# Kernel tuning notes

Hardware: AMD Instinct MI355X
Metric: run time of the kernel (lower is better)

## Reference

```python
import jax, jax.numpy as jnp
import numpy as np
import math

N_HEAD = 9
N_KV_HEAD = 3
HEAD_DIM = 64
ROPE_THETA = 100000.0


def _rope_cos_sin(seq_len, dim, theta):
    inv_freq = 1.0 / (theta ** (jnp.arange(0, dim, 2, dtype=jnp.float32) / dim))  # (dim//2,)
    t = jnp.arange(seq_len, dtype=jnp.float32)
    ang = jnp.outer(t, inv_freq)  # (T, dim//2)
    return jnp.cos(ang), jnp.sin(ang)


def _apply_rope(x, cos, sin):
    # x: (B, H, T, D); pairs are interleaved along D (torch view_as_complex on (..., D//2, 2))
    B, H, T, D = x.shape
    xr = x.reshape(B, H, T, D // 2, 2)
    x0, x1 = xr[..., 0], xr[..., 1]
    c = cos[None, None, :, :]
    s = sin[None, None, :, :]
    out0 = x0 * c - x1 * s
    out1 = x0 * s + x1 * c
    return jnp.stack([out0, out1], axis=-1).reshape(B, H, T, D)


def setup_inputs() -> dict:
    key = jax.random.key(0)
    ks = jax.random.split(key, 5)
    B, T, C = 4, 2048, 576
    scale_in = 1.0 / math.sqrt(C)
    return {
        "x": jax.random.normal(ks[0], (B, T, C), dtype=jnp.float32),
        "wq": jax.random.normal(ks[1], (N_HEAD * HEAD_DIM, C), dtype=jnp.float32) * scale_in,
        "wk": jax.random.normal(ks[2], (N_KV_HEAD * HEAD_DIM, C), dtype=jnp.float32) * scale_in,
        "wv": jax.random.normal(ks[3], (N_KV_HEAD * HEAD_DIM, C), dtype=jnp.float32) * scale_in,
        "wo": jax.random.normal(ks[4], (C, N_HEAD * HEAD_DIM), dtype=jnp.float32) * scale_in,
    }


def reference(x, wq, wk, wv, wo):
    B, T, C = x.shape
    n_rep = N_HEAD // N_KV_HEAD

    q = (x @ wq.T).reshape(B, T, N_HEAD, HEAD_DIM).transpose(0, 2, 1, 3)      # (B,Hq,T,D)
    k = (x @ wk.T).reshape(B, T, N_KV_HEAD, HEAD_DIM).transpose(0, 2, 1, 3)   # (B,Hkv,T,D)
    v = (x @ wv.T).reshape(B, T, N_KV_HEAD, HEAD_DIM).transpose(0, 2, 1, 3)

    cos, sin = _rope_cos_sin(T, HEAD_DIM, ROPE_THETA)
    q = _apply_rope(q, cos, sin)
    k = _apply_rope(k, cos, sin)

    # GQA: broadcast each KV head across n_rep query heads without materializing copies
    qg = q.reshape(B, N_KV_HEAD, n_rep, T, HEAD_DIM)
    att = jnp.einsum("bgrtd,bgsd->bgrts", qg, k) * (1.0 / math.sqrt(HEAD_DIM))  # (B,Hkv,rep,T,T)
    causal = jnp.tril(jnp.ones((T, T), dtype=bool))
    att = jnp.where(causal[None, None, None, :, :], att, -jnp.inf)
    att = jax.nn.softmax(att, axis=-1)
    y = jnp.einsum("bgrts,bgsd->bgrtd", att, v)                                # (B,Hkv,rep,T,D)
    y = y.reshape(B, N_HEAD, T, HEAD_DIM).transpose(0, 2, 1, 3).reshape(B, T, N_HEAD * HEAD_DIM)
    return y @ wo.T
```

## Files before the change

kernel.cpp:

```cpp
#include <hip/hip_runtime.h>
#include <stdint.h>

typedef __attribute__((ext_vector_type(8))) short bf16x8;
typedef __attribute__((ext_vector_type(16))) float f32x16;

#define MFMA32(a, b, c) __builtin_amdgcn_mfma_f32_32x32x16_bf16(a, b, c, 0, 0, 0)

#define BB 4
#define TT 2048
#define CC 576
#define NH 9
#define NKV 3
#define HD 64
#define MM (BB * TT)
#define NQKV 960

#define QSC 0.18033688011112042f

__device__ __forceinline__ unsigned short f2bf(float f) {
  union { float f; uint32_t u; } v; v.f = f;
  uint32_t u = v.u;
  uint32_t r = (u + 0x7fffu + ((u >> 16) & 1u)) >> 16;
  return (unsigned short)r;
}

__device__ __forceinline__ void gl16(const void* g, void* l) {
  __builtin_amdgcn_global_load_lds(
      (const __attribute__((address_space(1))) unsigned int*)g,
      (__attribute__((address_space(3))) unsigned int*)l, 16, 0, 0);
}

__device__ __forceinline__ float fexp2(float x) {
  float r;
  asm("v_exp_f32 %0, %1" : "=v"(r) : "v"(x));
  return r;
}

__global__ __launch_bounds__(256) void prep_kernel(
    const float* __restrict__ x, const float* __restrict__ wq,
    const float* __restrict__ wk, const float* __restrict__ wv,
    const float* __restrict__ wo,
    unsigned short* __restrict__ xh, unsigned short* __restrict__ wqkv,
    unsigned short* __restrict__ woh, float* __restrict__ tc,
    float* __restrict__ ts) {
  const int NX4 = MM * CC / 4;
  const int NW4 = NQKV * CC / 4;
  const int NO4 = CC * CC / 4;
  const int NT = TT * 32;
  const int total = NX4 + NW4 + NO4 + NT;
  for (int i = blockIdx.x * blockDim.x + threadIdx.x; i < total;
       i += gridDim.x * blockDim.x) {
    if (i < NX4) {
      float4 v = ((const float4*)x)[i];
      ushort4 o;
      o.x = f2bf(v.x); o.y = f2bf(v.y); o.z = f2bf(v.z); o.w = f2bf(v.w);
      ((ushort4*)xh)[i] = o;
    } else if (i < NX4 + NW4) {
      int j = i - NX4;
      int n = (j * 4) / CC;
      const float* src = (n < 576) ? wq + j * 4
                       : (n < 768) ? wk + j * 4 - 576 * CC
                                   : wv + j * 4 - 768 * CC;
      float4 v = *(const float4*)src;
      ushort4 o;
      o.x = f2bf(v.x); o.y = f2bf(v.y); o.z = f2bf(v.z); o.w = f2bf(v.w);
      ((ushort4*)wqkv)[j] = o;
    } else if (i < NX4 + NW4 + NO4) {
      int j = i - NX4 - NW4;
      float4 v = ((const float4*)wo)[j];
      ushort4 o;
      o.x = f2bf(v.x); o.y = f2bf(v.y); o.z = f2bf(v.z); o.w = f2bf(v.w);
      ((ushort4*)woh)[j] = o;
    } else {
      int j = i - NX4 - NW4 - NO4;
      int t = j >> 5, pi = j & 31;
      double invf = pow(100000.0, -(double)(2 * pi) / 64.0);
      double ang = (double)t * invf;
      tc[j] = (float)cos(ang);
      ts[j] = (float)sin(ang);
    }
  }
}

__global__ __launch_bounds__(256) void gemm_qkv(
    const unsigned short* __restrict__ xh, const unsigned short* __restrict__ wqkv,
    const float* __restrict__ tc, const float* __restrict__ ts,
    unsigned short* __restrict__ qb, unsigned short* __restrict__ kst,
    unsigned short* __restrict__ vst) {
  const int l = threadIdx.x & 63, w = threadIdx.x >> 6;
  const int ln = l & 31, hi = l >> 5;
  const int bm = blockIdx.y * 128, bn = blockIdx.x * 64;

  __shared__ unsigned short als[2][8192];
  __shared__ unsigned short bls[2][4096];

  int asrc[4], bsrc[2];
#pragma unroll
  for (int i = 0; i < 4; ++i)
    asrc[i] = (bm + w * 32 + i * 8 + (l >> 3)) * CC + ((l & 7) ^ ((l >> 3) & 7)) * 8;
#pragma unroll
  for (int i = 0; i < 2; ++i)
    bsrc[i] = (bn + w * 16 + i * 8 + (l >> 3)) * CC + ((l & 7) ^ ((l >> 3) & 7)) * 8;

  f32x16 acc0, acc1;
#pragma unroll
  for (int r = 0; r < 16; ++r) { acc0[r] = 0.f; acc1[r] = 0.f; }

#pragma unroll
  for (int i = 0; i < 4; ++i) gl16(xh + asrc[i], (char*)&als[0][0] + w * 4096 + i * 1024);
#pragma unroll
  for (int i = 0; i < 2; ++i) gl16(wqkv + bsrc[i], (char*)&bls[0][0] + w * 2048 + i * 1024);

  int cur = 0;
  for (int t = 0; t < 9; ++t) {
    if (t + 1 < 9) {
      const int k0 = (t + 1) * 64;
#pragma unroll
      for (int i = 0; i < 4; ++i)
        gl16(xh + asrc[i] + k0, (char*)&als[cur ^ 1][0] + w * 4096 + i * 1024);
#pragma unroll
      for (int i = 0; i < 2; ++i)
        gl16(wqkv + bsrc[i] + k0, (char*)&bls[cur ^ 1][0] + w * 2048 + i * 1024);
      asm volatile("s_waitcnt vmcnt(6)" ::: "memory");
    } else {
      asm volatile("s_waitcnt vmcnt(0)" ::: "memory");
    }
    __builtin_amdgcn_s_barrier();
    __builtin_amdgcn_sched_barrier(0);

    const char* ab = (const char*)&als[cur][0];
    const char* bb = (const char*)&bls[cur][0];
    __builtin_amdgcn_s_setprio(1);
#pragma unroll
    for (int ks = 0; ks < 4; ++ks) {
      const int ch = (((ks * 2 + hi) ^ (ln & 7)) << 4);
      bf16x8 af = *(const bf16x8*)(ab + (w * 32 + ln) * 128 + ch);
      bf16x8 b0 = *(const bf16x8*)(bb + ln * 128 + ch);
      bf16x8 b1 = *(const bf16x8*)(bb + (32 + ln) * 128 + ch);
      acc0 = MFMA32(af, b0, acc0);
      acc1 = MFMA32(af, b1, acc1);
    }
    __builtin_amdgcn_s_setprio(0);

    __builtin_amdgcn_sched_barrier(0);
    __builtin_amdgcn_s_barrier();
    cur ^= 1;
  }

#pragma unroll
  for (int n32 = 0; n32 < 2; ++n32) {
    const int col = bn + n32 * 32 + ln;
    const int d = col & 63;
#pragma unroll
    for (int r = 0; r < 16; ++r) {
      const int m = bm + w * 32 + (r & 3) + 8 * (r >> 2) + 4 * hi;
      float v = n32 ? acc1[r] : acc0[r];
      float partner = __shfl_xor(v, 1);
      const int bi = m >> 11, t = m & 2047;
      if (col < 768) {
        const int pi = d >> 1;
        const float c = tc[t * 32 + pi], s = ts[t * 32 + pi];
        v = (d & 1) ? (partner * s + v * c) : (v * c - partner * s);
      }
      if (col < 576) {
        const int h = col >> 6;
        qb[(((size_t)bi * NH + h) * TT + t) * HD + d] = f2bf(v * QSC);
      } else if (col < 768) {
        const int h = (col - 576) >> 6;
        const size_t head = (size_t)bi * NKV + h;
        kst[((head * 32 + (t >> 6)) * 64 + (t & 63)) * 64 + (d ^ ((t & 7) << 3))] = f2bf(v);
      } else {
        const int h = (col - 768) >> 6;
        const size_t head = (size_t)bi * NKV + h;
        vst[((head * 32 + (t >> 6)) * 64 + d) * 64 + ((t & 63) ^ ((d & 7) << 3))] = f2bf(v);
      }
    }
  }
}

__global__ __launch_bounds__(512) void attn_kernel(
    const unsigned short* __restrict__ qbuf, const unsigned short* __restrict__ kst,
    const unsigned short* __restrict__ vst, unsigned short* __restrict__ yb) {
  const int j = blockIdx.x, kvh = blockIdx.y, b = blockIdx.z;
  const int i = j % 7, hr = j / 7;
  const int h = kvh * 3 + hr;
  const int l = threadIdx.x & 63;
  const int w8 = threadIdx.x >> 6;
  const int g = w8 >> 2;
  const int wq = w8 & 3;
  const int ln = l & 31, hi = l >> 5;
  const size_t head = (size_t)b * NKV + kvh;

  const int qt0 = 15 - i, qt1 = i + 2, qt2 = (i == 5) ? 0 : 1;
  const int m0 = qt0 + 1, m1 = qt1 + 1;
  const int m2 = (i >= 5) ? qt2 + 1 : 0;
  const int m01 = m0 + m1;
  const int tot = m01 + m2;

  __shared__ unsigned short kls[2][3][4096];
  __shared__ unsigned short vls[2][3][4096];
  __shared__ float licomb[256];

  const unsigned short* qptr = qbuf + ((size_t)b * NH + h) * TT * HD;
  const int row0 = qt0 * 128 + wq * 32 + ln;
  const int row1 = qt1 * 128 + wq * 32 + ln;
  const int row2 = qt2 * 128 + wq * 32 + ln;

  bf16x8 qf0[4], qf1[4], qf2[4], qc[4];
#pragma unroll
  for (int ds = 0; ds < 4; ++ds) {
    qf0[ds] = *(const bf16x8*)(qptr + (size_t)row0 * HD + ds * 16 + hi * 8);
    qf1[ds] = *(const bf16x8*)(qptr + (size_t)row1 * HD + ds * 16 + hi * 8);
    qf2[ds] = *(const bf16x8*)(qptr + (size_t)row2 * HD + ds * 16 + hi * 8);
  }
  qc[0] = qf0[0]; qc[1] = qf0[1]; qc[2] = qf0[2]; qc[3] = qf0[3];
  int qt_c = qt0, qrow_c = row0, nt_c = m0;

  const char* kgb = (const char*)(kst + head * 32 * 4096);
  const char* vgb = (const char*)(vst + head * 32 * 4096);

  f32x16 o0, o1, fzero;
  float ls[16];
#pragma unroll
  for (int r = 0; r < 16; ++r) { o0[r] = 0.f; o1[r] = 0.f; ls[r] = 0.f; fzero[r] = 0.f; }

#pragma unroll
  for (int pre = 0; pre < 2; ++pre) {
    const size_t tb = (size_t)(2 * pre + g) * 8192;
#pragma unroll
    for (int i2 = 0; i2 < 2; ++i2) {
      const int off = wq * 2048 + i2 * 1024;
      gl16(kgb + tb + off + l * 16, (char*)&kls[g][pre][0] + off);
      gl16(vgb + tb + off + l * 16, (char*)&vls[g][pre][0] + off);
    }
  }
  asm volatile("s_waitcnt vmcnt(4)" ::: "memory");
  __builtin_amdgcn_s_barrier();
  __builtin_amdgcn_sched_barrier(0);

  const int swz = (ln & 7) << 4;
  int jt = 0;
  int s = 0;

  for (int it = 0; it < tot; ++it) {
    if (it + 2 < tot) {
      const int f = it + 2;
      const int u2 = (f < m0) ? f : ((f < m01) ? f - m0 : f - m01);
      const size_t tb = (size_t)(2 * u2 + g) * 8192;
      char* kl = (char*)&kls[g][(it + 2) % 3][0];
      char* vl = (char*)&vls[g][(it + 2) % 3][0];
#pragma unroll
      for (int i2 = 0; i2 < 2; ++i2) {
        const int off = wq * 2048 + i2 * 1024;
        gl16(kgb + tb + off + l * 16, kl + off);
        gl16(vgb + tb + off + l * 16, vl + off);
      }
    }

    const char* kb = (const char*)&kls[g][it % 3][0];
    const char* vb = (const char*)&vls[g][it % 3][0];

    f32x16 s0, s1;
    __builtin_amdgcn_s_setprio(1);
    {
      const int cb0 = (hi * 16) ^ swz;
      bf16x8 k0 = *(const bf16x8*)(kb + ln * 128 + cb0);
      bf16x8 k1 = *(const bf16x8*)(kb + (32 + ln) * 128 + cb0);
      s0 = MFMA32(k0, qc[0], fzero);
      s1 = MFMA32(k1, qc[0], fzero);
    }
#pragma unroll
    for (int ds = 1; ds < 4; ++ds) {
      const int cb = (ds * 32 + hi * 16) ^ swz;
      bf16x8 k0 = *(const bf16x8*)(kb + ln * 128 + cb);
      bf16x8 k1 = *(const bf16x8*)(kb + (32 + ln) * 128 + cb);
      s0 = MFMA32(k0, qc[ds], s0);
      s1 = MFMA32(k1, qc[ds], s1);
    }
    __builtin_amdgcn_s_setprio(0);

    const bool segEnd = (jt == qt_c);
    if (segEnd) {
      const int kvt = 2 * qt_c + g;
#pragma unroll
      for (int r = 0; r < 16; ++r) {
        const int kg = kvt * 64 + (r & 3) + 8 * (r >> 2) + 4 * hi;
        if (kg > qrow_c) s0[r] = -1e30f;
        if (kg + 32 > qrow_c) s1[r] = -1e30f;
      }
    }

#pragma unroll
    for (int r = 0; r < 16; ++r) {
      s0[r] = fexp2(s0[r]);
      s1[r] = fexp2(s1[r]);
    }
#pragma unroll
    for (int r = 0; r < 16; ++r) ls[r] += s0[r] + s1[r];

    unsigned int pa[4][4];
#pragma unroll
    for (int t = 0; t < 2; ++t) {
#pragma unroll
      for (int m = 0; m < 2; ++m) {
        float p0 = t ? s1[8 * m + 0] : s0[8 * m + 0];
        float p1 = t ? s1[8 * m + 1] : s0[8 * m + 1];
        float p2 = t ? s1[8 * m + 2] : s0[8 * m + 2];
        float p3 = t ? s1[8 * m + 3] : s0[8 * m + 3];
        float p4 = t ? s1[8 * m + 4] : s0[8 * m + 4];
        float p5 = t ? s1[8 * m + 5] : s0[8 * m + 5];
        float p6 = t ? s1[8 * m + 6] : s0[8 * m + 6];
        float p7 = t ? s1[8 * m + 7] : s0[8 * m + 7];
        unsigned int w0, w1, w2, w3;
        asm("v_cvt_pk_bf16_f32 %0, %1, %2" : "=v"(w0) : "v"(p0), "v"(p1));
        asm("v_cvt_pk_bf16_f32 %0, %1, %2" : "=v"(w1) : "v"(p2), "v"(p3));
        asm("v_cvt_pk_bf16_f32 %0, %1, %2" : "=v"(w2) : "v"(p4), "v"(p5));
        asm("v_cvt_pk_bf16_f32 %0, %1, %2" : "=v"(w3) : "v"(p6), "v"(p7));
        asm("v_permlane32_swap_b32 %0, %1" : "+v"(w0), "+v"(w2));
        asm("v_permlane32_swap_b32 %0, %1" : "+v"(w1), "+v"(w3));
        pa[2 * t + m][0] = w0; pa[2 * t + m][1] = w1;
        pa[2 * t + m][2] = w2; pa[2 * t + m][3] = w3;
      }
    }

    __builtin_amdgcn_s_setprio(1);
#pragma unroll
    for (int ks = 0; ks < 4; ++ks) {
      union { unsigned int u[4]; bf16x8 v; } cvt;
      cvt.u[0] = pa[ks][0]; cvt.u[1] = pa[ks][1];
      cvt.u[2] = pa[ks][2]; cvt.u[3] = pa[ks][3];
      const int cb = (ks * 32 + hi * 16) ^ swz;
      bf16x8 v0 = *(const bf16x8*)(vb + ln * 128 + cb);
      bf16x8 v1 = *(const bf16x8*)(vb + (32 + ln) * 128 + cb);
      o0 = MFMA32(cvt.v, v0, o0);
      o1 = MFMA32(cvt.v, v1, o1);
    }
    __builtin_amdgcn_s_setprio(0);

    if (segEnd) {
      float tm0 = 0.f;
#pragma unroll
      for (int st = 8; st >= 1; st >>= 1)
#pragma unroll
        for (int r = 0; r < 8; ++r)
          if (r < st) ls[r] += ls[r + st];
      tm0 = ls[0] + __shfl_xor(ls[0], 32);
      char* chunk;
      {
        const int buf = it % 3;
        chunk = (char*)((wq == 0) ? &kls[0][buf][0]
               : (wq == 1) ? &vls[0][buf][0]
               : (wq == 2) ? &kls[1][buf][0]
                           : &vls[1][buf][0]);
      }
      __syncthreads();
      if (g == 1) {
#pragma unroll
        for (int r = 0; r < 16; ++r) {
          *(float*)(chunk + r * 256 + l * 4) = o0[r];
          *(float*)(chunk + (16 + r) * 256 + l * 4) = o1[r];
        }
        licomb[wq * 64 + l] = tm0;
      }
      __syncthreads();
      if (g == 0) {
#pragma unroll
        for (int r = 0; r < 16; ++r) {
          o0[r] += *(const float*)(chunk + r * 256 + l * 4);
          o1[r] += *(const float*)(chunk + (16 + r) * 256 + l * 4);
        }
        const float li = tm0 + licomb[wq * 64 + l];
        const float inv = 1.0f / li;
#pragma unroll
        for (int r = 0; r < 16; ++r) {
          const int cr = (r & 3) + 8 * (r >> 2) + 4 * hi;
          const float ir = __shfl(inv, cr);
          const int t = qt_c * 128 + wq * 32 + cr;
          unsigned short* yp = yb + ((size_t)b * TT + t) * CC + h * HD;
          yp[ln] = f2bf(o0[r] * ir);
          yp[32 + ln] = f2bf(o1[r] * ir);
        }
      }
#pragma unroll
      for (int r = 0; r < 16; ++r) { o0[r] = 0.f; o1[r] = 0.f; ls[r] = 0.f; }
    }

    __builtin_amdgcn_sched_barrier(0);
    if (it + 2 < tot) {
      asm volatile("s_waitcnt vmcnt(4)" ::: "memory");
    } else {
      asm volatile("s_waitcnt vmcnt(0)" ::: "memory");
    }
    __builtin_amdgcn_s_barrier();
    __builtin_amdgcn_sched_barrier(0);

    ++jt;
    if (jt == nt_c) {
      jt = 0; ++s;
      if (s == 1) {
        qt_c = qt1; qrow_c = row1; nt_c = m1;
        qc[0] = qf1[0]; qc[1] = qf1[1]; qc[2] = qf1[2]; qc[3] = qf1[3];
      } else {
        qt_c = qt2; qrow_c = row2; nt_c = m2;
        qc[0] = qf2[0]; qc[1] = qf2[1]; qc[2] = qf2[2]; qc[3] = qf2[3];
      }
    }
  }
}

__global__ __launch_bounds__(256) void gemm_out(
    const unsigned short* __restrict__ yb, const unsigned short* __restrict__ woh,
    float* __restrict__ out) {
  const int l = threadIdx.x & 63, w = threadIdx.x >> 6;
  const int ln = l & 31, hi = l >> 5;
  const int bm = blockIdx.y * 128, bn = blockIdx.x * 64;

  __shared__ unsigned short als[2][8192];
  __shared__ unsigned short bls[2][4096];

  int asrc[4], bsrc[2];
#pragma unroll
  for (int i = 0; i < 4; ++i)
    asrc[i] = (bm + w * 32 + i * 8 + (l >> 3)) * CC + ((l & 7) ^ ((l >> 3) & 7)) * 8;
#pragma unroll
  for (int i = 0; i < 2; ++i)
    bsrc[i] = (bn + w * 16 + i * 8 + (l >> 3)) * CC + ((l & 7) ^ ((l >> 3) & 7)) * 8;

  f32x16 acc0, acc1;
#pragma unroll
  for (int r = 0; r < 16; ++r) { acc0[r] = 0.f; acc1[r] = 0.f; }

#pragma unroll
  for (int i = 0; i < 4; ++i) gl16(yb + asrc[i], (char*)&als[0][0] + w * 4096 + i * 1024);
#pragma unroll
  for (int i = 0; i < 2; ++i) gl16(woh + bsrc[i], (char*)&bls[0][0] + w * 2048 + i * 1024);

  int cur = 0;
  for (int t = 0; t < 9; ++t) {
    if (t + 1 < 9) {
      const int k0 = (t + 1) * 64;
#pragma unroll
      for (int i = 0; i < 4; ++i)
        gl16(yb + asrc[i] + k0, (char*)&als[cur ^ 1][0] + w * 4096 + i * 1024);
#pragma unroll
      for (int i = 0; i < 2; ++i)
        gl16(woh + bsrc[i] + k0, (char*)&bls[cur ^ 1][0] + w * 2048 + i * 1024);
      asm volatile("s_waitcnt vmcnt(6)" ::: "memory");
    } else {
      asm volatile("s_waitcnt vmcnt(0)" ::: "memory");
    }
    __builtin_amdgcn_s_barrier();
    __builtin_amdgcn_sched_barrier(0);

    const char* ab = (const char*)&als[cur][0];
    const char* bb = (const char*)&bls[cur][0];
    __builtin_amdgcn_s_setprio(1);
#pragma unroll
    for (int ks = 0; ks < 4; ++ks) {
      const int ch = (((ks * 2 + hi) ^ (ln & 7)) << 4);
      bf16x8 af = *(const bf16x8*)(ab + (w * 32 + ln) * 128 + ch);
      bf16x8 b0 = *(const bf16x8*)(bb + ln * 128 + ch);
      bf16x8 b1 = *(const bf16x8*)(bb + (32 + ln) * 128 + ch);
      acc0 = MFMA32(af, b0, acc0);
      acc1 = MFMA32(af, b1, acc1);
    }
    __builtin_amdgcn_s_setprio(0);

    __builtin_amdgcn_sched_barrier(0);
    __builtin_amdgcn_s_barrier();
    cur ^= 1;
  }

#pragma unroll
  for (int n32 = 0; n32 < 2; ++n32) {
    const int col = bn + n32 * 32 + ln;
#pragma unroll
    for (int r = 0; r < 16; ++r) {
      const int m = bm + w * 32 + (r & 3) + 8 * (r >> 2) + 4 * hi;
      out[(size_t)m * CC + col] = n32 ? acc1[r] : acc0[r];
    }
  }
}

extern "C" void kernel_launch(void* const* d_in, const int* in_sizes, int n_in,
                              void* d_out, int out_size, void* d_ws, size_t ws_size,
                              hipStream_t stream) {
  const float* x = (const float*)d_in[0];
  const float* wq = (const float*)d_in[1];
  const float* wk = (const float*)d_in[2];
  const float* wv = (const float*)d_in[3];
  const float* wo = (const float*)d_in[4];
  float* out = (float*)d_out;

  char* ws = (char*)d_ws;
  unsigned short* xh = (unsigned short*)ws;    ws += (size_t)MM * CC * 2;
  unsigned short* wqkv = (unsigned short*)ws;  ws += (size_t)NQKV * CC * 2;
  unsigned short* woh = (unsigned short*)ws;   ws += (size_t)CC * CC * 2;
  float* tc = (float*)ws;                      ws += (size_t)TT * 32 * 4;
  float* tsn = (float*)ws;                     ws += (size_t)TT * 32 * 4;
  unsigned short* qbuf = (unsigned short*)ws;  ws += (size_t)BB * NH * TT * HD * 2;
  unsigned short* kst = (unsigned short*)ws;   ws += (size_t)BB * NKV * TT * HD * 2;
  unsigned short* vst = (unsigned short*)ws;   ws += (size_t)BB * NKV * HD * TT * 2;
  unsigned short* yb = (unsigned short*)ws;    ws += (size_t)MM * CC * 2;

  prep_kernel<<<dim3(2048), dim3(256), 0, stream>>>(x, wq, wk, wv, wo, xh, wqkv, woh, tc, tsn);
  gemm_qkv<<<dim3(NQKV / 64, MM / 128), dim3(256), 0, stream>>>(xh, wqkv, tc, tsn, qbuf, kst, vst);
  attn_kernel<<<dim3(21, NKV, BB), dim3(512), 0, stream>>>(qbuf, kst, vst, yb);
  gemm_out<<<dim3(CC / 64, MM / 128), dim3(256), 0, stream>>>(yb, woh, out);
}
```

Before: 109.3 us.

## Double query rows per attention wave and enlarge GEMM tiles to 256 rows

The attention kernel now has each wave process two 32-row query sub-tiles against every K/V tile, so each K/V tile loaded into LDS is reused twice. Work per block becomes a balanced pair of 256-row query tiles, launched as 12 blocks per head group instead of 21. Both GEMMs move to 512-thread blocks with 256-row M tiles, so each block loads B with a single instruction per thread. The costs are higher register pressure from four accumulators per wave in attention, fewer blocks overall, and a two-phase cross-group combine at segment ends that needs extra barriers.

Result: no change. 111.2 us (+1.7%).

```diff
diff --git a/kernel.cpp b/kernel.cpp
--- a/kernel.cpp
+++ b/kernel.cpp
@@ -82,25 +82,23 @@
   }
 }
 
-__global__ __launch_bounds__(256) void gemm_qkv(
+__global__ __launch_bounds__(512, 4) void gemm_qkv(
     const unsigned short* __restrict__ xh, const unsigned short* __restrict__ wqkv,
     const float* __restrict__ tc, const float* __restrict__ ts,
     unsigned short* __restrict__ qb, unsigned short* __restrict__ kst,
     unsigned short* __restrict__ vst) {
   const int l = threadIdx.x & 63, w = threadIdx.x >> 6;
   const int ln = l & 31, hi = l >> 5;
-  const int bm = blockIdx.y * 128, bn = blockIdx.x * 64;
-
-  __shared__ unsigned short als[2][8192];
+  const int bm = blockIdx.y * 256, bn = blockIdx.x * 64;
+
+  __shared__ unsigned short als[2][16384];
   __shared__ unsigned short bls[2][4096];
 
-  int asrc[4], bsrc[2];
+  int asrc[4];
 #pragma unroll
   for (int i = 0; i < 4; ++i)
     asrc[i] = (bm + w * 32 + i * 8 + (l >> 3)) * CC + ((l & 7) ^ ((l >> 3) & 7)) * 8;
-#pragma unroll
-  for (int i = 0; i < 2; ++i)
-    bsrc[i] = (bn + w * 16 + i * 8 + (l >> 3)) * CC + ((l & 7) ^ ((l >> 3) & 7)) * 8;
+  const int bsrc = (bn + w * 8 + (l >> 3)) * CC + ((l & 7) ^ ((l >> 3) & 7)) * 8;
 
   f32x16 acc0, acc1;
 #pragma unroll
@@ -108,8 +106,7 @@
 
 #pragma unroll
   for (int i = 0; i < 4; ++i) gl16(xh + asrc[i], (char*)&als[0][0] + w * 4096 + i * 1024);
-#pragma unroll
-  for (int i = 0; i < 2; ++i) gl16(wqkv + bsrc[i], (char*)&bls[0][0] + w * 2048 + i * 1024);
+  gl16(wqkv + bsrc, (char*)&bls[0][0] + w * 1024);
 
   int cur = 0;
   for (int t = 0; t < 9; ++t) {
@@ -118,10 +115,8 @@
 #pragma unroll
       for (int i = 0; i < 4; ++i)
         gl16(xh + asrc[i] + k0, (char*)&als[cur ^ 1][0] + w * 4096 + i * 1024);
-#pragma unroll
-      for (int i = 0; i < 2; ++i)
-        gl16(wqkv + bsrc[i] + k0, (char*)&bls[cur ^ 1][0] + w * 2048 + i * 1024);
-      asm volatile("s_waitcnt vmcnt(6)" ::: "memory");
+      gl16(wqkv + bsrc + k0, (char*)&bls[cur ^ 1][0] + w * 1024);
+      asm volatile("s_waitcnt vmcnt(5)" ::: "memory");
     } else {
       asm volatile("s_waitcnt vmcnt(0)" ::: "memory");
     }
@@ -178,11 +173,11 @@
   }
 }
 
-__global__ __launch_bounds__(512) void attn_kernel(
+__global__ __launch_bounds__(512, 2) void attn_kernel(
     const unsigned short* __restrict__ qbuf, const unsigned short* __restrict__ kst,
     const unsigned short* __restrict__ vst, unsigned short* __restrict__ yb) {
   const int j = blockIdx.x, kvh = blockIdx.y, b = blockIdx.z;
-  const int i = j % 7, hr = j / 7;
+  const int i = j & 3, hr = j >> 2;
   const int h = kvh * 3 + hr;
   const int l = threadIdx.x & 63;
   const int w8 = threadIdx.x >> 6;
@@ -191,38 +186,34 @@
   const int ln = l & 31, hi = l >> 5;
   const size_t head = (size_t)b * NKV + kvh;
 
-  const int qt0 = 15 - i, qt1 = i + 2, qt2 = (i == 5) ? 0 : 1;
-  const int m0 = qt0 + 1, m1 = qt1 + 1;
-  const int m2 = (i >= 5) ? qt2 + 1 : 0;
-  const int m01 = m0 + m1;
-  const int tot = m01 + m2;
+  const int qt0 = 7 - i, qt1 = i;
+  const int m0 = 2 * qt0 + 2, m1 = 2 * qt1 + 2;
+  const int tot = m0 + m1;
 
   __shared__ unsigned short kls[2][3][4096];
   __shared__ unsigned short vls[2][3][4096];
   __shared__ float licomb[256];
 
   const unsigned short* qptr = qbuf + ((size_t)b * NH + h) * TT * HD;
-  const int row0 = qt0 * 128 + wq * 32 + ln;
-  const int row1 = qt1 * 128 + wq * 32 + ln;
-  const int row2 = qt2 * 128 + wq * 32 + ln;
-
-  bf16x8 qf0[4], qf1[4], qf2[4], qc[4];
+
+  int qrA = qt0 * 256 + wq * 64 + ln;
+  bf16x8 qa[4], qb_[4];
 #pragma unroll
   for (int ds = 0; ds < 4; ++ds) {
-    qf0[ds] = *(const bf16x8*)(qptr + (size_t)row0 * HD + ds * 16 + hi * 8);
-    qf1[ds] = *(const bf16x8*)(qptr + (size_t)row1 * HD + ds * 16 + hi * 8);
-    qf2[ds] = *(const bf16x8*)(qptr + (size_t)row2 * HD + ds * 16 + hi * 8);
-  }
-  qc[0] = qf0[0]; qc[1] = qf0[1]; qc[2] = qf0[2]; qc[3] = qf0[3];
-  int qt_c = qt0, qrow_c = row0, nt_c = m0;
+    qa[ds]  = *(const bf16x8*)(qptr + (size_t)qrA * HD + ds * 16 + hi * 8);
+    qb_[ds] = *(const bf16x8*)(qptr + (size_t)(qrA + 32) * HD + ds * 16 + hi * 8);
+  }
+  int qt_c = qt0, nt_c = m0;
 
   const char* kgb = (const char*)(kst + head * 32 * 4096);
   const char* vgb = (const char*)(vst + head * 32 * 4096);
 
-  f32x16 o0, o1, fzero;
-  float ls[16];
-#pragma unroll
-  for (int r = 0; r < 16; ++r) { o0[r] = 0.f; o1[r] = 0.f; ls[r] = 0.f; fzero[r] = 0.f; }
+  f32x16 oA0, oA1, oB0, oB1, fzero;
+  float lsA[4], lsB[4];
+#pragma unroll
+  for (int r = 0; r < 16; ++r) { oA0[r] = 0.f; oA1[r] = 0.f; oB0[r] = 0.f; oB1[r] = 0.f; fzero[r] = 0.f; }
+#pragma unroll
+  for (int r = 0; r < 4; ++r) { lsA[r] = 0.f; lsB[r] = 0.f; }
 
 #pragma unroll
   for (int pre = 0; pre < 2; ++pre) {
@@ -240,12 +231,11 @@
 
   const int swz = (ln & 7) << 4;
   int jt = 0;
-  int s = 0;
 
   for (int it = 0; it < tot; ++it) {
     if (it + 2 < tot) {
       const int f = it + 2;
-      const int u2 = (f < m0) ? f : ((f < m01) ? f - m0 : f - m01);
+      const int u2 = (f < m0) ? f : f - m0;
       const size_t tb = (size_t)(2 * u2 + g) * 8192;
       char* kl = (char*)&kls[g][(it + 2) % 3][0];
       char* vl = (char*)&vls[g][(it + 2) % 3][0];
@@ -259,130 +249,197 @@
 
     const char* kb = (const char*)&kls[g][it % 3][0];
     const char* vb = (const char*)&vls[g][it % 3][0];
-
-    f32x16 s0, s1;
+    const int kvt = 2 * jt + g;
+
+    f32x16 sA0, sA1, sB0, sB1;
     __builtin_amdgcn_s_setprio(1);
     {
       const int cb0 = (hi * 16) ^ swz;
       bf16x8 k0 = *(const bf16x8*)(kb + ln * 128 + cb0);
       bf16x8 k1 = *(const bf16x8*)(kb + (32 + ln) * 128 + cb0);
-      s0 = MFMA32(k0, qc[0], fzero);
-      s1 = MFMA32(k1, qc[0], fzero);
+      sA0 = MFMA32(k0, qa[0], fzero);
+      sB0 = MFMA32(k0, qb_[0], fzero);
+      sA1 = MFMA32(k1, qa[0], fzero);
+      sB1 = MFMA32(k1, qb_[0], fzero);
     }
 #pragma unroll
     for (int ds = 1; ds < 4; ++ds) {
       const int cb = (ds * 32 + hi * 16) ^ swz;
       bf16x8 k0 = *(const bf16x8*)(kb + ln * 128 + cb);
       bf16x8 k1 = *(const bf16x8*)(kb + (32 + ln) * 128 + cb);
-      s0 = MFMA32(k0, qc[ds], s0);
-      s1 = MFMA32(k1, qc[ds], s1);
+      sA0 = MFMA32(k0, qa[ds], sA0);
+      sB0 = MFMA32(k0, qb_[ds], sB0);
+      sA1 = MFMA32(k1, qa[ds], sA1);
+      sB1 = MFMA32(k1, qb_[ds], sB1);
     }
     __builtin_amdgcn_s_setprio(0);
 
-    const bool segEnd = (jt == qt_c);
-    if (segEnd) {
-      const int kvt = 2 * qt_c + g;
+    if (jt >= nt_c - 2) {
 #pragma unroll
       for (int r = 0; r < 16; ++r) {
         const int kg = kvt * 64 + (r & 3) + 8 * (r >> 2) + 4 * hi;
-        if (kg > qrow_c) s0[r] = -1e30f;
-        if (kg + 32 > qrow_c) s1[r] = -1e30f;
+        if (kg > qrA) sA0[r] = -1e30f;
+        if (kg + 32 > qrA) sA1[r] = -1e30f;
+        if (kg > qrA + 32) sB0[r] = -1e30f;
+        if (kg + 32 > qrA + 32) sB1[r] = -1e30f;
       }
     }
 
 #pragma unroll
     for (int r = 0; r < 16; ++r) {
-      s0[r] = fexp2(s0[r]);
-      s1[r] = fexp2(s1[r]);
-    }
-#pragma unroll
-    for (int r = 0; r < 16; ++r) ls[r] += s0[r] + s1[r];
-
-    unsigned int pa[4][4];
+      sA0[r] = fexp2(sA0[r]); sA1[r] = fexp2(sA1[r]);
+      sB0[r] = fexp2(sB0[r]); sB1[r] = fexp2(sB1[r]);
+    }
+#pragma unroll
+    for (int r = 0; r < 16; ++r) {
+      lsA[r & 3] += sA0[r] + sA1[r];
+      lsB[r & 3] += sB0[r] + sB1[r];
+    }
+
+    unsigned int paA[4][4], paB[4][4];
 #pragma unroll
     for (int t = 0; t < 2; ++t) {
 #pragma unroll
       for (int m = 0; m < 2; ++m) {
-        float p0 = t ? s1[8 * m + 0] : s0[8 * m + 0];
-        float p1 = t ? s1[8 * m + 1] : s0[8 * m + 1];
-        float p2 = t ? s1[8 * m + 2] : s0[8 * m + 2];
-        float p3 = t ? s1[8 * m + 3] : s0[8 * m + 3];
-        float p4 = t ? s1[8 * m + 4] : s0[8 * m + 4];
-        float p5 = t ? s1[8 * m + 5] : s0[8 * m + 5];
-        float p6 = t ? s1[8 * m + 6] : s0[8 * m + 6];
-        float p7 = t ? s1[8 * m + 7] : s0[8 * m + 7];
-        unsigned int w0, w1, w2, w3;
-        asm("v_cvt_pk_bf16_f32 %0, %1, %2" : "=v"(w0) : "v"(p0), "v"(p1));
-        asm("v_cvt_pk_bf16_f32 %0, %1, %2" : "=v"(w1) : "v"(p2), "v"(p3));
-        asm("v_cvt_pk_bf16_f32 %0, %1, %2" : "=v"(w2) : "v"(p4), "v"(p5));
-        asm("v_cvt_pk_bf16_f32 %0, %1, %2" : "=v"(w3) : "v"(p6), "v"(p7));
-        asm("v_permlane32_swap_b32 %0, %1" : "+v"(w0), "+v"(w2));
-        asm("v_permlane32_swap_b32 %0, %1" : "+v"(w1), "+v"(w3));
-        pa[2 * t + m][0] = w0; pa[2 * t + m][1] = w1;
-        pa[2 * t + m][2] = w2; pa[2 * t + m][3] = w3;
+        {
+          float p0 = t ? sA1[8 * m + 0] : sA0[8 * m + 0];
+          float p1 = t ? sA1[8 * m + 1] : sA0[8 * m + 1];
+          float p2 = t ? sA1[8 * m + 2] : sA0[8 * m + 2];
+          float p3 = t ? sA1[8 * m + 3] : sA0[8 * m + 3];
+          float p4 = t ? sA1[8 * m + 4] : sA0[8 * m + 4];
+          float p5 = t ? sA1[8 * m + 5] : sA0[8 * m + 5];
+          float p6 = t ? sA1[8 * m + 6] : sA0[8 * m + 6];
+          float p7 = t ? sA1[8 * m + 7] : sA0[8 * m + 7];
+          unsigned int w0, w1, w2, w3;
+          asm("v_cvt_pk_bf16_f32 %0, %1, %2" : "=v"(w0) : "v"(p0), "v"(p1));
+          asm("v_cvt_pk_bf16_f32 %0, %1, %2" : "=v"(w1) : "v"(p2), "v"(p3));
+          asm("v_cvt_pk_bf16_f32 %0, %1, %2" : "=v"(w2) : "v"(p4), "v"(p5));
+          asm("v_cvt_pk_bf16_f32 %0, %1, %2" : "=v"(w3) : "v"(p6), "v"(p7));
+          asm("v_permlane32_swap_b32 %0, %1" : "+v"(w0), "+v"(w2));
+          asm("v_permlane32_swap_b32 %0, %1" : "+v"(w1), "+v"(w3));
+          paA[2 * t + m][0] = w0; paA[2 * t + m][1] = w1;
+          paA[2 * t + m][2] = w2; paA[2 * t + m][3] = w3;
+        }
+        {
+          float p0 = t ? sB1[8 * m + 0] : sB0[8 * m + 0];
+          float p1 = t ? sB1[8 * m + 1] : sB0[8 * m + 1];
+          float p2 = t ? sB1[8 * m + 2] : sB0[8 * m + 2];
+          float p3 = t ? sB1[8 * m + 3] : sB0[8 * m + 3];
+          float p4 = t ? sB1[8 * m + 4] : sB0[8 * m + 4];
+          float p5 = t ? sB1[8 * m + 5] : sB0[8 * m + 5];
+          float p6 = t ? sB1[8 * m + 6] : sB0[8 * m + 6];
+          float p7 = t ? sB1[8 * m + 7] : sB0[8 * m + 7];
+          unsigned int w0, w1, w2, w3;
+          asm("v_cvt_pk_bf16_f32 %0, %1, %2" : "=v"(w0) : "v"(p0), "v"(p1));
+          asm("v_cvt_pk_bf16_f32 %0, %1, %2" : "=v"(w1) : "v"(p2), "v"(p3));
+          asm("v_cvt_pk_bf16_f32 %0, %1, %2" : "=v"(w2) : "v"(p4), "v"(p5));
+          asm("v_cvt_pk_bf16_f32 %0, %1, %2" : "=v"(w3) : "v"(p6), "v"(p7));
+          asm("v_permlane32_swap_b32 %0, %1" : "+v"(w0), "+v"(w2));
+          asm("v_permlane32_swap_b32 %0, %1" : "+v"(w1), "+v"(w3));
+          paB[2 * t + m][0] = w0; paB[2 * t + m][1] = w1;
+          paB[2 * t + m][2] = w2; paB[2 * t + m][3] = w3;
+        }
       }
     }
 
     __builtin_amdgcn_s_setprio(1);
 #pragma unroll
     for (int ks = 0; ks < 4; ++ks) {
-      union { unsigned int u[4]; bf16x8 v; } cvt;
-      cvt.u[0] = pa[ks][0]; cvt.u[1] = pa[ks][1];
-      cvt.u[2] = pa[ks][2]; cvt.u[3] = pa[ks][3];
+      union { unsigned int u[4]; bf16x8 v; } ca, cb2;
+      ca.u[0] = paA[ks][0]; ca.u[1] = paA[ks][1];
+      ca.u[2] = paA[ks][2]; ca.u[3] = paA[ks][3];
+      cb2.u[0] = paB[ks][0]; cb2.u[1] = paB[ks][1];
+      cb2.u[2] = paB[ks][2]; cb2.u[3] = paB[ks][3];
       const int cb = (ks * 32 + hi * 16) ^ swz;
       bf16x8 v0 = *(const bf16x8*)(vb + ln * 128 + cb);
       bf16x8 v1 = *(const bf16x8*)(vb + (32 + ln) * 128 + cb);
-      o0 = MFMA32(cvt.v, v0, o0);
-      o1 = MFMA32(cvt.v, v1, o1);
+      oA0 = MFMA32(ca.v, v0, oA0);
+      oB0 = MFMA32(cb2.v, v0, oB0);
+      oA1 = MFMA32(ca.v, v1, oA1);
+      oB1 = MFMA32(cb2.v, v1, oB1);
     }
     __builtin_amdgcn_s_setprio(0);
 
-    if (segEnd) {
-      float tm0 = 0.f;
-#pragma unroll
-      for (int st = 8; st >= 1; st >>= 1)
-#pragma unroll
-        for (int r = 0; r < 8; ++r)
-          if (r < st) ls[r] += ls[r + st];
-      tm0 = ls[0] + __shfl_xor(ls[0], 32);
-      char* chunk;
-      {
-        const int buf = it % 3;
-        chunk = (char*)((wq == 0) ? &kls[0][buf][0]
-               : (wq == 1) ? &vls[0][buf][0]
-               : (wq == 2) ? &kls[1][buf][0]
-                           : &vls[1][buf][0]);
-      }
-      __syncthreads();
+    if (jt == nt_c - 1) {
+      float lA = (lsA[0] + lsA[1]) + (lsA[2] + lsA[3]);
+      lA += __shfl_xor(lA, 32);
+      float lB = (lsB[0] + lsB[1]) + (lsB[2] + lsB[3]);
+      lB += __shfl_xor(lB, 32);
+      const int buf = it % 3;
+      char* chunk = (char*)((wq == 0) ? &kls[0][buf][0]
+                   : (wq == 1) ? &vls[0][buf][0]
+                   : (wq == 2) ? &kls[1][buf][0]
+                               : &vls[1][buf][0]);
+      __builtin_amdgcn_sched_barrier(0);
+      __builtin_amdgcn_s_barrier();
       if (g == 1) {
 #pragma unroll
         for (int r = 0; r < 16; ++r) {
-          *(float*)(chunk + r * 256 + l * 4) = o0[r];
-          *(float*)(chunk + (16 + r) * 256 + l * 4) = o1[r];
-        }
-        licomb[wq * 64 + l] = tm0;
-      }
-      __syncthreads();
+          *(float*)(chunk + r * 256 + l * 4) = oA0[r];
+          *(float*)(chunk + (16 + r) * 256 + l * 4) = oA1[r];
+        }
+        licomb[wq * 64 + l] = lA;
+      }
+      asm volatile("s_waitcnt lgkmcnt(0)" ::: "memory");
+      __builtin_amdgcn_s_barrier();
       if (g == 0) {
 #pragma unroll
         for (int r = 0; r < 16; ++r) {
-          o0[r] += *(const float*)(chunk + r * 256 + l * 4);
-          o1[r] += *(const float*)(chunk + (16 + r) * 256 + l * 4);
-        }
-        const float li = tm0 + licomb[wq * 64 + l];
-        const float inv = 1.0f / li;
+          oA0[r] += *(const float*)(chunk + r * 256 + l * 4);
+          oA1[r] += *(const float*)(chunk + (16 + r) * 256 + l * 4);
+        }
+        const float inv = 1.0f / (lA + licomb[wq * 64 + l]);
 #pragma unroll
         for (int r = 0; r < 16; ++r) {
           const int cr = (r & 3) + 8 * (r >> 2) + 4 * hi;
           const float ir = __shfl(inv, cr);
-          const int t = qt_c * 128 + wq * 32 + cr;
+          const int t = qt_c * 256 + wq * 64 + cr;
           unsigned short* yp = yb + ((size_t)b * TT + t) * CC + h * HD;
-          yp[ln] = f2bf(o0[r] * ir);
-          yp[32 + ln] = f2bf(o1[r] * ir);
-        }
-      }
-#pragma unroll
-      for (int r = 0; r < 16; ++r) { o0[r] = 0.f; o1[r] = 0.f; ls[r] = 0.f; }
+          yp[ln] = f2bf(oA0[r] * ir);
+          yp[32 + ln] = f2bf(oA1[r] * ir);
+        }
+      }
+      __builtin_amdgcn_s_barrier();
+      if (g == 1) {
+#pragma unroll
+        for (int r = 0; r < 16; ++r) {
+          *(float*)(chunk + r * 256 + l * 4) = oB0[r];
+          *(float*)(chunk + (16 + r) * 256 + l * 4) = oB1[r];
+        }
+        licomb[wq * 64 + l] = lB;
+      }
+      asm volatile("s_waitcnt lgkmcnt(0)" ::: "memory");
+      __builtin_amdgcn_s_barrier();
+      if (g == 0) {
+#pragma unroll
+        for (int r = 0; r < 16; ++r) {
+          oB0[r] += *(const float*)(chunk + r * 256 + l * 4);
+          oB1[r] += *(const float*)(chunk + (16 + r) * 256 + l * 4);
+        }
+        const float inv = 1.0f / (lB + licomb[wq * 64 + l]);
+#pragma unroll
+        for (int r = 0; r < 16; ++r) {
+          const int cr = (r & 3) + 8 * (r >> 2) + 4 * hi;
+          const float ir = __shfl(inv, cr);
+          const int t = qt_c * 256 + wq * 64 + 32 + cr;
+          unsigned short* yp = yb + ((size_t)b * TT + t) * CC + h * HD;
+          yp[ln] = f2bf(oB0[r] * ir);
+          yp[32 + ln] = f2bf(oB1[r] * ir);
+        }
+      }
+      oA0 = fzero; oA1 = fzero; oB0 = fzero; oB1 = fzero;
+#pragma unroll
+      for (int r = 0; r < 4; ++r) { lsA[r] = 0.f; lsB[r] = 0.f; }
+      if (it + 1 < tot) {
+        qt_c = qt1; nt_c = m1;
+        qrA = qt1 * 256 + wq * 64 + ln;
+#pragma unroll
+        for (int ds = 0; ds < 4; ++ds) {
+          qa[ds]  = *(const bf16x8*)(qptr + (size_t)qrA * HD + ds * 16 + hi * 8);
+          qb_[ds] = *(const bf16x8*)(qptr + (size_t)(qrA + 32) * HD + ds * 16 + hi * 8);
+        }
+        jt = -1;
+      }
     }
 
     __builtin_amdgcn_sched_barrier(0);
@@ -393,38 +450,25 @@
     }
     __builtin_amdgcn_s_barrier();
     __builtin_amdgcn_sched_barrier(0);
-
     ++jt;
-    if (jt == nt_c) {
-      jt = 0; ++s;
-      if (s == 1) {
-        qt_c = qt1; qrow_c = row1; nt_c = m1;
-        qc[0] = qf1[0]; qc[1] = qf1[1]; qc[2] = qf1[2]; qc[3] = qf1[3];
-      } else {
-        qt_c = qt2; qrow_c = row2; nt_c = m2;
-        qc[0] = qf2[0]; qc[1] = qf2[1]; qc[2] = qf2[2]; qc[3] = qf2[3];
-      }
-    }
-  }
-}
-
-__global__ __launch_bounds__(256) void gemm_out(
+  }
+}
+
+__global__ __launch_bounds__(512, 4) void gemm_out(
     const unsigned short* __restrict__ yb, const unsigned short* __restrict__ woh,
     float* __restrict__ out) {
   const int l = threadIdx.x & 63, w = threadIdx.x >> 6;
   const int ln = l & 31, hi = l >> 5;
-  const int bm = blockIdx.y * 128, bn = blockIdx.x * 64;
-
-  __shared__ unsigned short als[2][8192];
+  const int bm = blockIdx.y * 256, bn = blockIdx.x * 64;
+
+  __shared__ unsigned short als[2][16384];
   __shared__ unsigned short bls[2][4096];
 
-  int asrc[4], bsrc[2];
+  int asrc[4];
 #pragma unroll
   for (int i = 0; i < 4; ++i)
     asrc[i] = (bm + w * 32 + i * 8 + (l >> 3)) * CC + ((l & 7) ^ ((l >> 3) & 7)) * 8;
-#pragma unroll
-  for (int i = 0; i < 2; ++i)
-    bsrc[i] = (bn + w * 16 + i * 8 + (l >> 3)) * CC + ((l & 7) ^ ((l >> 3) & 7)) * 8;
+  const int bsrc = (bn + w * 8 + (l >> 3)) * CC + ((l & 7) ^ ((l >> 3) & 7)) * 8;
 
   f32x16 acc0, acc1;
 #pragma unroll
@@ -432,8 +476,7 @@
 
 #pragma unroll
   for (int i = 0; i < 4; ++i) gl16(yb + asrc[i], (char*)&als[0][0] + w * 4096 + i * 1024);
-#pragma unroll
-  for (int i = 0; i < 2; ++i) gl16(woh + bsrc[i], (char*)&bls[0][0] + w * 2048 + i * 1024);
+  gl16(woh + bsrc, (char*)&bls[0][0] + w * 1024);
 
   int cur = 0;
   for (int t = 0; t < 9; ++t) {
@@ -442,10 +485,8 @@
 #pragma unroll
       for (int i = 0; i < 4; ++i)
         gl16(yb + asrc[i] + k0, (char*)&als[cur ^ 1][0] + w * 4096 + i * 1024);
-#pragma unroll
-      for (int i = 0; i < 2; ++i)
-        gl16(woh + bsrc[i] + k0, (char*)&bls[cur ^ 1][0] + w * 2048 + i * 1024);
-      asm volatile("s_waitcnt vmcnt(6)" ::: "memory");
+      gl16(woh + bsrc + k0, (char*)&bls[cur ^ 1][0] + w * 1024);
+      asm volatile("s_waitcnt vmcnt(5)" ::: "memory");
     } else {
       asm volatile("s_waitcnt vmcnt(0)" ::: "memory");
     }
@@ -504,7 +545,7 @@
   unsigned short* yb = (unsigned short*)ws;    ws += (size_t)MM * CC * 2;
 
   prep_kernel<<<dim3(2048), dim3(256), 0, stream>>>(x, wq, wk, wv, wo, xh, wqkv, woh, tc, tsn);
-  gemm_qkv<<<dim3(NQKV / 64, MM / 128), dim3(256), 0, stream>>>(xh, wqkv, tc, tsn, qbuf, kst, vst);
-  attn_kernel<<<dim3(21, NKV, BB), dim3(512), 0, stream>>>(qbuf, kst, vst, yb);
-  gemm_out<<<dim3(CC / 64, MM / 128), dim3(256), 0, stream>>>(yb, woh, out);
-}
+  gemm_qkv<<<dim3(NQKV / 64, MM / 256), dim3(512), 0, stream>>>(xh, wqkv, tc, tsn, qbuf, kst, vst);
+  attn_kernel<<<dim3(12, NKV, BB), dim3(512), 0, stream>>>(qbuf, kst, vst, yb);
+  gemm_out<<<dim3(CC / 64, MM / 256), dim3(512), 0, stream>>>(yb, woh, out);
+}
```

## Store K/V in MFMA-fragment order and enlarge GEMM tiles to 256 rows

Applied to the files above, without the earlier changes.

K and V are now written by the QKV GEMM epilogue directly in per-lane MFMA operand order. Attention can then load each operand with a contiguous l*16 LDS read instead of swizzled row addressing. Separately, both GEMMs use 512-thread blocks covering 256 rows of M, so each B tile is loaded once per 256 rows and each wave issues one B global load instead of two. The larger blocks use more LDS per block and launch half as many blocks, which may reduce how well the work spreads across CUs.

Measured after the change: 100.2 us. 8.4% less time.

```diff
diff --git a/kernel.cpp b/kernel.cpp
--- a/kernel.cpp
+++ b/kernel.cpp
@@ -82,25 +82,23 @@
   }
 }
 
-__global__ __launch_bounds__(256) void gemm_qkv(
+__global__ __launch_bounds__(512, 4) void gemm_qkv(
     const unsigned short* __restrict__ xh, const unsigned short* __restrict__ wqkv,
     const float* __restrict__ tc, const float* __restrict__ ts,
     unsigned short* __restrict__ qb, unsigned short* __restrict__ kst,
     unsigned short* __restrict__ vst) {
   const int l = threadIdx.x & 63, w = threadIdx.x >> 6;
   const int ln = l & 31, hi = l >> 5;
-  const int bm = blockIdx.y * 128, bn = blockIdx.x * 64;
-
-  __shared__ unsigned short als[2][8192];
+  const int bm = blockIdx.y * 256, bn = blockIdx.x * 64;
+
+  __shared__ unsigned short als[2][16384];
   __shared__ unsigned short bls[2][4096];
 
-  int asrc[4], bsrc[2];
+  int asrc[4];
 #pragma unroll
   for (int i = 0; i < 4; ++i)
     asrc[i] = (bm + w * 32 + i * 8 + (l >> 3)) * CC + ((l & 7) ^ ((l >> 3) & 7)) * 8;
-#pragma unroll
-  for (int i = 0; i < 2; ++i)
-    bsrc[i] = (bn + w * 16 + i * 8 + (l >> 3)) * CC + ((l & 7) ^ ((l >> 3) & 7)) * 8;
+  const int bsrc = (bn + w * 8 + (l >> 3)) * CC + ((l & 7) ^ ((l >> 3) & 7)) * 8;
 
   f32x16 acc0, acc1;
 #pragma unroll
@@ -108,8 +106,7 @@
 
 #pragma unroll
   for (int i = 0; i < 4; ++i) gl16(xh + asrc[i], (char*)&als[0][0] + w * 4096 + i * 1024);
-#pragma unroll
-  for (int i = 0; i < 2; ++i) gl16(wqkv + bsrc[i], (char*)&bls[0][0] + w * 2048 + i * 1024);
+  gl16(wqkv + bsrc, (char*)&bls[0][0] + w * 1024);
 
   int cur = 0;
   for (int t = 0; t < 9; ++t) {
@@ -118,10 +115,8 @@
 #pragma unroll
       for (int i = 0; i < 4; ++i)
         gl16(xh + asrc[i] + k0, (char*)&als[cur ^ 1][0] + w * 4096 + i * 1024);
-#pragma unroll
-      for (int i = 0; i < 2; ++i)
-        gl16(wqkv + bsrc[i] + k0, (char*)&bls[cur ^ 1][0] + w * 2048 + i * 1024);
-      asm volatile("s_waitcnt vmcnt(6)" ::: "memory");
+      gl16(wqkv + bsrc + k0, (char*)&bls[cur ^ 1][0] + w * 1024);
+      asm volatile("s_waitcnt vmcnt(5)" ::: "memory");
     } else {
       asm volatile("s_waitcnt vmcnt(0)" ::: "memory");
     }
@@ -168,11 +163,15 @@
       } else if (col < 768) {
         const int h = (col - 576) >> 6;
         const size_t head = (size_t)bi * NKV + h;
-        kst[((head * 32 + (t >> 6)) * 64 + (t & 63)) * 64 + (d ^ ((t & 7) << 3))] = f2bf(v);
+        const int tt = t & 63;
+        kst[(head * 32 + (t >> 6)) * 4096 + ((d >> 4) * 2 + (tt >> 5)) * 512
+            + ((((d >> 3) & 1) << 5) + (tt & 31)) * 8 + (d & 7)] = f2bf(v);
       } else {
         const int h = (col - 768) >> 6;
         const size_t head = (size_t)bi * NKV + h;
-        vst[((head * 32 + (t >> 6)) * 64 + d) * 64 + ((t & 63) ^ ((d & 7) << 3))] = f2bf(v);
+        const int tt = t & 63;
+        vst[(head * 32 + (t >> 6)) * 4096 + ((tt >> 4) * 2 + (d >> 5)) * 512
+            + ((((tt >> 3) & 1) << 5) + (d & 31)) * 8 + (tt & 7)] = f2bf(v);
       }
     }
   }
@@ -238,7 +237,6 @@
   __builtin_amdgcn_s_barrier();
   __builtin_amdgcn_sched_barrier(0);
 
-  const int swz = (ln & 7) << 4;
   int jt = 0;
   int s = 0;
 
@@ -263,17 +261,15 @@
     f32x16 s0, s1;
     __builtin_amdgcn_s_setprio(1);
     {
-      const int cb0 = (hi * 16) ^ swz;
-      bf16x8 k0 = *(const bf16x8*)(kb + ln * 128 + cb0);
-      bf16x8 k1 = *(const bf16x8*)(kb + (32 + ln) * 128 + cb0);
+      bf16x8 k0 = *(const bf16x8*)(kb + 0 * 1024 + l * 16);
+      bf16x8 k1 = *(const bf16x8*)(kb + 1 * 1024 + l * 16);
       s0 = MFMA32(k0, qc[0], fzero);
       s1 = MFMA32(k1, qc[0], fzero);
     }
 #pragma unroll
     for (int ds = 1; ds < 4; ++ds) {
-      const int cb = (ds * 32 + hi * 16) ^ swz;
-      bf16x8 k0 = *(const bf16x8*)(kb + ln * 128 + cb);
-      bf16x8 k1 = *(const bf16x8*)(kb + (32 + ln) * 128 + cb);
+      bf16x8 k0 = *(const bf16x8*)(kb + (ds * 2 + 0) * 1024 + l * 16);
+      bf16x8 k1 = *(const bf16x8*)(kb + (ds * 2 + 1) * 1024 + l * 16);
       s0 = MFMA32(k0, qc[ds], s0);
       s1 = MFMA32(k1, qc[ds], s1);
     }
@@ -329,22 +325,20 @@
       union { unsigned int u[4]; bf16x8 v; } cvt;
       cvt.u[0] = pa[ks][0]; cvt.u[1] = pa[ks][1];
       cvt.u[2] = pa[ks][2]; cvt.u[3] = pa[ks][3];
-      const int cb = (ks * 32 + hi * 16) ^ swz;
-      bf16x8 v0 = *(const bf16x8*)(vb + ln * 128 + cb);
-      bf16x8 v1 = *(const bf16x8*)(vb + (32 + ln) * 128 + cb);
+      bf16x8 v0 = *(const bf16x8*)(vb + (ks * 2 + 0) * 1024 + l * 16);
+      bf16x8 v1 = *(const bf16x8*)(vb + (ks * 2 + 1) * 1024 + l * 16);
       o0 = MFMA32(cvt.v, v0, o0);
       o1 = MFMA32(cvt.v, v1, o1);
     }
     __builtin_amdgcn_s_setprio(0);
 
     if (segEnd) {
-      float tm0 = 0.f;
 #pragma unroll
       for (int st = 8; st >= 1; st >>= 1)
 #pragma unroll
         for (int r = 0; r < 8; ++r)
           if (r < st) ls[r] += ls[r + st];
-      tm0 = ls[0] + __shfl_xor(ls[0], 32);
+      const float tm0 = ls[0] + __shfl_xor(ls[0], 32);
       char* chunk;
       {
         const int buf = it % 3;
@@ -408,23 +402,21 @@
   }
 }
 
-__global__ __launch_bounds__(256) void gemm_out(
+__global__ __launch_bounds__(512, 4) void gemm_out(
     const unsigned short* __restrict__ yb, const unsigned short* __restrict__ woh,
     float* __restrict__ out) {
   const int l = threadIdx.x & 63, w = threadIdx.x >> 6;
   const int ln = l & 31, hi = l >> 5;
-  const int bm = blockIdx.y * 128, bn = blockIdx.x * 64;
-
-  __shared__ unsigned short als[2][8192];
+  const int bm = blockIdx.y * 256, bn = blockIdx.x * 64;
+
+  __shared__ unsigned short als[2][16384];
   __shared__ unsigned short bls[2][4096];
 
-  int asrc[4], bsrc[2];
+  int asrc[4];
 #pragma unroll
   for (int i = 0; i < 4; ++i)
     asrc[i] = (bm + w * 32 + i * 8 + (l >> 3)) * CC + ((l & 7) ^ ((l >> 3) & 7)) * 8;
-#pragma unroll
-  for (int i = 0; i < 2; ++i)
-    bsrc[i] = (bn + w * 16 + i * 8 + (l >> 3)) * CC + ((l & 7) ^ ((l >> 3) & 7)) * 8;
+  const int bsrc = (bn + w * 8 + (l >> 3)) * CC + ((l & 7) ^ ((l >> 3) & 7)) * 8;
 
   f32x16 acc0, acc1;
 #pragma unroll
@@ -432,8 +424,7 @@
 
 #pragma unroll
   for (int i = 0; i < 4; ++i) gl16(yb + asrc[i], (char*)&als[0][0] + w * 4096 + i * 1024);
-#pragma unroll
-  for (int i = 0; i < 2; ++i) gl16(woh + bsrc[i], (char*)&bls[0][0] + w * 2048 + i * 1024);
+  gl16(woh + bsrc, (char*)&bls[0][0] + w * 1024);
 
   int cur = 0;
   for (int t = 0; t < 9; ++t) {
@@ -442,10 +433,8 @@
 #pragma unroll
       for (int i = 0; i < 4; ++i)
         gl16(yb + asrc[i] + k0, (char*)&als[cur ^ 1][0] + w * 4096 + i * 1024);
-#pragma unroll
-      for (int i = 0; i < 2; ++i)
-        gl16(woh + bsrc[i] + k0, (char*)&bls[cur ^ 1][0] + w * 2048 + i * 1024);
-      asm volatile("s_waitcnt vmcnt(6)" ::: "memory");
+      gl16(woh + bsrc + k0, (char*)&bls[cur ^ 1][0] + w * 1024);
+      asm volatile("s_waitcnt vmcnt(5)" ::: "memory");
     } else {
       asm volatile("s_waitcnt vmcnt(0)" ::: "memory");
     }
@@ -504,7 +493,7 @@
   unsigned short* yb = (unsigned short*)ws;    ws += (size_t)MM * CC * 2;
 
   prep_kernel<<<dim3(2048), dim3(256), 0, stream>>>(x, wq, wk, wv, wo, xh, wqkv, woh, tc, tsn);
-  gemm_qkv<<<dim3(NQKV / 64, MM / 128), dim3(256), 0, stream>>>(xh, wqkv, tc, tsn, qbuf, kst, vst);
+  gemm_qkv<<<dim3(NQKV / 64, MM / 256), dim3(512), 0, stream>>>(xh, wqkv, tc, tsn, qbuf, kst, vst);
   attn_kernel<<<dim3(21, NKV, BB), dim3(512), 0, stream>>>(qbuf, kst, vst, yb);
-  gemm_out<<<dim3(CC / 64, MM / 128), dim3(256), 0, stream>>>(yb, woh, out);
-}
+  gemm_out<<<dim3(CC / 64, MM / 256), dim3(512), 0, stream>>>(yb, woh, out);
+}
```
